# Kernel tuning notes

Measured on AMD Instinct MI355X. Metric: run time of the kernel, lower is better.

## Reference

```python
import jax, jax.numpy as jnp
import numpy as np

NUM_CAMS = 4
E = 256          # embed_dim
H_HEADS = 8      # num_heads
DH = E // H_HEADS
CIN = 64
FF = 4 * E
N_LAYERS = 2
EPS = 1e-5


def _layer_norm(x, g, b):
    mu = jnp.mean(x, axis=-1, keepdims=True)
    var = jnp.mean((x - mu) ** 2, axis=-1, keepdims=True)
    return (x - mu) * jax.lax.rsqrt(var + EPS) * g + b


def setup_inputs() -> dict:
    key = jax.random.key(0)
    ks = jax.random.split(key, 20)
    s = 0.02
    inp = {
        "features": jax.random.normal(ks[0], (NUM_CAMS, 2, CIN, 96, 96), jnp.float32),
        # 1x1 input projection conv
        "Wp": jax.random.normal(ks[1], (E, CIN), jnp.float32) * s,
        "bp": jnp.zeros((E,), jnp.float32),
        # per-layer attention params (stacked over 2 layers)
        "Wqkv": jax.random.normal(ks[2], (N_LAYERS, 3 * E, E), jnp.float32) * s,
        "bqkv": jnp.zeros((N_LAYERS, 3 * E), jnp.float32),
        "Wo": jax.random.normal(ks[3], (N_LAYERS, E, E), jnp.float32) * s,
        "bo": jnp.zeros((N_LAYERS, E), jnp.float32),
        # FFN
        "W1": jax.random.normal(ks[4], (N_LAYERS, FF, E), jnp.float32) * s,
        "b1": jnp.zeros((N_LAYERS, FF), jnp.float32),
        "W2": jax.random.normal(ks[5], (N_LAYERS, E, FF), jnp.float32) * s,
        "b2": jnp.zeros((N_LAYERS, E), jnp.float32),
        # LayerNorms
        "g1": jnp.ones((N_LAYERS, E), jnp.float32),
        "be1": jnp.zeros((N_LAYERS, E), jnp.float32),
        "g2": jnp.ones((N_LAYERS, E), jnp.float32),
        "be2": jnp.zeros((N_LAYERS, E), jnp.float32),
        # 1x1 output conv
        "Wout": jax.random.normal(ks[6], (CIN, E), jnp.float32) * s,
        "bout": jnp.zeros((CIN,), jnp.float32),
    }
    return inp


def reference(features, Wp, bp, Wqkv, bqkv, Wo, bo, W1, b1, W2, b2,
              g1, be1, g2, be2, Wout, bout):
    n_cam, B, Cin, Hh, Ww = features.shape
    # 1x1 conv projection + rearrange to per-pixel sequences: [B*H*W, n_cam, E]
    x = jnp.einsum('nbchw,ec->bhwne', features, Wp) + bp
    x = x.reshape(B * Hh * Ww, n_cam, E)

    scale = 1.0 / jnp.sqrt(jnp.float32(DH))
    for i in range(N_LAYERS):
        # self-attention (post-norm encoder layer, dropout=identity in eval)
        qkv = x @ Wqkv[i].T + bqkv[i]                      # [N, S, 3E]
        q, k, v = jnp.split(qkv, 3, axis=-1)
        q = q.reshape(-1, n_cam, H_HEADS, DH)
        k = k.reshape(-1, n_cam, H_HEADS, DH)
        v = v.reshape(-1, n_cam, H_HEADS, DH)
        scores = jnp.einsum('nqhd,nkhd->nhqk', q, k) * scale
        attn = jax.nn.softmax(scores, axis=-1)
        sa = jnp.einsum('nhqk,nkhd->nqhd', attn, v).reshape(-1, n_cam, E)
        sa = sa @ Wo[i].T + bo[i]
        x = _layer_norm(x + sa, g1[i], be1[i])
        # FFN (ReLU activation, default)
        ff = jax.nn.relu(x @ W1[i].T + b1[i]) @ W2[i].T + b2[i]
        x = _layer_norm(x + ff, g2[i], be2[i])

    # mean over cameras, back to [B, C, H, W] via 1x1 output conv
    fused = x.mean(axis=1).reshape(B, Hh, Ww, E)
    out = jnp.einsum('bhwe,ce->bchw', fused, Wout) + bout[None, :, None, None]
    return out
```

## Files before the change

### kernel.cpp

```cpp
#include <hip/hip_runtime.h>
#include <cstdint>
#include <cstddef>


typedef __bf16 bf16;
typedef __bf16 bf16x8 __attribute__((ext_vector_type(8)));
typedef __bf16 bf16x4 __attribute__((ext_vector_type(4)));
typedef float  f32x4  __attribute__((ext_vector_type(4)));

__device__ __forceinline__ void async_copy16(const void* g, void* l)
{
    __builtin_amdgcn_global_load_lds(
        (__attribute__((address_space(1))) void*)g,
        (__attribute__((address_space(3))) void*)l,
        16, 0, 0);
}

__global__ void pack_all_k(const float* __restrict__ s0, const float* __restrict__ s1,
                           const float* __restrict__ s2, const float* __restrict__ s3,
                           const float* __restrict__ s4,
                           bf16* __restrict__ d0, bf16* __restrict__ d1,
                           bf16* __restrict__ d2, bf16* __restrict__ d3,
                           bf16* __restrict__ d4)
{
    const int i = blockIdx.x * 256 + threadIdx.x;
    if (i < 393216)       d0[i] = (bf16)s0[i];
    else if (i < 524288)  d1[i - 393216] = (bf16)s1[i - 393216];
    else if (i < 1048576) d2[i - 524288] = (bf16)s2[i - 524288];
    else if (i < 1572864) d3[i - 1048576] = (bf16)s3[i - 1048576];
    else                  d4[i - 1572864] = (bf16)s4[i - 1572864];
}

__global__ __launch_bounds__(256) void feat_pack_k(const float* __restrict__ feat,
                                                   bf16* __restrict__ Xf)
{
    __shared__ float ft[64][68];

    const int tid  = threadIdx.x;
    const int camb = blockIdx.y;
    const int cam  = camb >> 1;
    const int b    = camb & 1;
    const int hw0  = blockIdx.x * 64;

    const float* fb = feat + (size_t)camb * 64 * 9216 + hw0;
#pragma unroll
    for (int rep = 0; rep < 16; ++rep) {
        const int idx = rep * 256 + tid;
        const int c = idx >> 6, p = idx & 63;
        ft[p][c] = fb[(size_t)c * 9216 + p];
    }
    __syncthreads();

    const int pbase = b * 9216 + hw0;
#pragma unroll
    for (int rep = 0; rep < 2; ++rep) {
        const int idx = rep * 256 + tid;
        const int p = idx >> 3, cc = idx & 7;
        const f32x4 a = *(const f32x4*)(&ft[p][cc * 8]);
        const f32x4 c4 = *(const f32x4*)(&ft[p][cc * 8 + 4]);
        bf16x8 v;
#pragma unroll
        for (int i = 0; i < 4; ++i) { v[i] = (bf16)a[i]; v[4 + i] = (bf16)c4[i]; }
        const size_t t = (size_t)(pbase + p) * 4 + cam;
        *(bf16x8*)(Xf + t * 64 + cc * 8) = v;
    }
}

template <bool RELU>
__global__ __launch_bounds__(256, 2) void gemm_bt(
    const bf16* __restrict__ A, const bf16* __restrict__ B,
    const float* __restrict__ bias, bf16* __restrict__ C,
    int N, int K)
{
    __shared__ __align__(16) bf16 As[128 * 64];
    __shared__ __align__(16) bf16 Bs[128 * 64];

    const int tid  = threadIdx.x;
    const int lane = tid & 63;
    const int wv   = tid >> 6;
    const int wm   = wv >> 1;
    const int wn   = wv & 1;
    const int bm   = blockIdx.y * 128;
    const int bn   = blockIdx.x * 128;

    const int r8  = lane >> 3;
    const int p8  = lane & 7;
    const int gch = p8 ^ r8;

    const int quad = lane >> 4;
    const int l16  = lane & 15;

    f32x4 acc[4][4] = {};

    for (int k0 = 0; k0 < K; k0 += 64) {
#pragma unroll
        for (int inst = 0; inst < 4; ++inst) {
            const int row = wv * 32 + inst * 8 + r8;
            const bf16* ga = A + (size_t)(bm + row) * K + (k0 + gch * 8);
            const bf16* gb = B + (size_t)(bn + row) * K + (k0 + gch * 8);
            async_copy16(ga, (char*)As + (wv * 4 + inst) * 1024);
            async_copy16(gb, (char*)Bs + (wv * 4 + inst) * 1024);
        }
        __syncthreads();

#pragma unroll
        for (int kk = 0; kk < 2; ++kk) {
            bf16x8 af[4], bfr[4];
            const int lch = kk * 4 + quad;
#pragma unroll
            for (int i = 0; i < 4; ++i) {
                const int m = wm * 64 + i * 16 + l16;
                af[i] = *(const bf16x8*)((const char*)As + (m * 8 + (lch ^ (m & 7))) * 16);
                const int n = wn * 64 + i * 16 + l16;
                bfr[i] = *(const bf16x8*)((const char*)Bs + (n * 8 + (lch ^ (n & 7))) * 16);
            }
#pragma unroll
            for (int i = 0; i < 4; ++i)
#pragma unroll
                for (int j = 0; j < 4; ++j)
                    acc[i][j] = __builtin_amdgcn_mfma_f32_16x16x32_bf16(
                        af[i], bfr[j], acc[i][j], 0, 0, 0);
        }
        __syncthreads();
    }

#pragma unroll
    for (int j = 0; j < 4; ++j) {
        const int n = bn + wn * 64 + j * 16 + l16;
        const float bv = bias[n];
#pragma unroll
        for (int i = 0; i < 4; ++i) {
            const int mb = bm + wm * 64 + i * 16 + quad * 4;
#pragma unroll
            for (int r = 0; r < 4; ++r) {
                float v = acc[i][j][r] + bv;
                if (RELU) v = fmaxf(v, 0.f);
                C[(size_t)(mb + r) * N + n] = (bf16)v;
            }
        }
    }
}

__global__ __launch_bounds__(256, 2) void gemm_ln_k(
    const bf16* __restrict__ A, const bf16* __restrict__ B,
    const float* __restrict__ bias, const bf16* __restrict__ Xres,
    const float* __restrict__ gam, const float* __restrict__ bet,
    bf16* __restrict__ Xout, int K)
{
    __shared__ __align__(16) bf16 S[24576];
    __shared__ float2 red[128][2];

    const int tid  = threadIdx.x;
    const int lane = tid & 63;
    const int wv   = tid >> 6;
    const int wm   = wv >> 1;
    const int wn   = wv & 1;
    const int bm   = blockIdx.x * 128;
    const int quad = lane >> 4;
    const int l16  = lane & 15;

    f32x4 acc[4][8] = {};

    for (int k0 = 0; k0 < K; k0 += 64) {
#pragma unroll
        for (int s = 0; s < 12; ++s) {
            const int L   = s * 256 + tid;
            const int row = L >> 3;
            const int gch = (L & 7) ^ (row & 7);
            const bf16* g = (row < 128)
                ? A + (size_t)(bm + row) * K + (k0 + gch * 8)
                : B + (size_t)(row - 128) * K + (k0 + gch * 8);
            async_copy16(g, (char*)S + (size_t)L * 16);
        }
        __syncthreads();

#pragma unroll
        for (int kk = 0; kk < 2; ++kk) {
            const int lch = kk * 4 + quad;
            bf16x8 af[4], bfr[8];
#pragma unroll
            for (int i = 0; i < 4; ++i) {
                const int m = wm * 64 + i * 16 + l16;
                af[i] = *(const bf16x8*)((const char*)S + (m * 8 + (lch ^ (m & 7))) * 16);
            }
#pragma unroll
            for (int j = 0; j < 8; ++j) {
                const int n = wn * 128 + j * 16 + l16;
                bfr[j] = *(const bf16x8*)((const char*)S + ((128 + n) * 8 + (lch ^ (n & 7))) * 16);
            }
#pragma unroll
            for (int i = 0; i < 4; ++i)
#pragma unroll
                for (int j = 0; j < 8; ++j)
                    acc[i][j] = __builtin_amdgcn_mfma_f32_16x16x32_bf16(
                        af[i], bfr[j], acc[i][j], 0, 0, 0);
        }
        __syncthreads();
    }

    float bv[8], gv[8], bev[8];
#pragma unroll
    for (int j = 0; j < 8; ++j) {
        const int n = wn * 128 + j * 16 + l16;
        bv[j] = bias[n]; gv[j] = gam[n]; bev[j] = bet[n];
    }

#pragma unroll
    for (int i = 0; i < 4; ++i) {
#pragma unroll
        for (int r = 0; r < 4; ++r) {
            const int rl  = wm * 64 + i * 16 + quad * 4 + r;
            const size_t row = (size_t)(bm + rl);
            float s1 = 0.f, s2 = 0.f;
#pragma unroll
            for (int j = 0; j < 8; ++j) {
                const int n = wn * 128 + j * 16 + l16;
                const float v = acc[i][j][r] + bv[j] + (float)Xres[row * 256 + n];
                acc[i][j][r] = v;
                s1 += v; s2 += v * v;
            }
#pragma unroll
            for (int off = 1; off < 16; off <<= 1) {
                s1 += __shfl_xor(s1, off, 64);
                s2 += __shfl_xor(s2, off, 64);
            }
            if (l16 == 0) red[rl][wn] = make_float2(s1, s2);
        }
    }
    __syncthreads();

#pragma unroll
    for (int i = 0; i < 4; ++i) {
#pragma unroll
        for (int r = 0; r < 4; ++r) {
            const int rl = wm * 64 + i * 16 + quad * 4 + r;
            const float2 p0 = red[rl][0], p1 = red[rl][1];
            const float mu  = (p0.x + p1.x) * (1.f / 256.f);
            const float ex2 = (p0.y + p1.y) * (1.f / 256.f);
            const float rstd = rsqrtf(fmaxf(ex2 - mu * mu, 0.f) + 1e-5f);
            const size_t row = (size_t)(bm + rl);
#pragma unroll
            for (int j = 0; j < 8; ++j) {
                const int n = wn * 128 + j * 16 + l16;
                Xout[row * 256 + n] = (bf16)((acc[i][j][r] - mu) * rstd * gv[j] + bev[j]);
            }
        }
    }
}

__device__ __forceinline__ void ffn_stage(int s, const bf16* __restrict__ W1,
                                          const bf16* __restrict__ W2,
                                          char* buf, int tid)
{
    const int hc = s >> 3;
    const int q  = s & 7;
    if (q < 4) {
#pragma unroll
        for (int it = 0; it < 4; ++it) {
            const int L = it * 256 + tid;
            const int row = L >> 3, psl = L & 7;
            const int c = psl ^ (row & 7);
            async_copy16(W1 + (size_t)(hc * 128 + row) * 256 + q * 64 + c * 8,
                         buf + (size_t)L * 16);
        }
    } else {
#pragma unroll
        for (int it = 0; it < 4; ++it) {
            const int L = it * 256 + tid;
            const int r128 = L >> 3, psl = L & 7;
            const int g = psl ^ (r128 & 7);
            const int n = r128 * 2 + (g >> 2);
            const int c = g & 3;
            async_copy16(W2 + (size_t)n * 1024 + hc * 128 + (q - 4) * 32 + c * 8,
                         buf + (size_t)L * 16);
        }
    }
}

__global__ __launch_bounds__(256, 2) void ffn_fused_k(
    const bf16* __restrict__ X,
    const bf16* __restrict__ W1, const float* __restrict__ b1,
    const bf16* __restrict__ W2, const float* __restrict__ b2,
    const float* __restrict__ gam, const float* __restrict__ bet,
    bf16* __restrict__ Xout)
{
    __shared__ __align__(16) char smem[81920];
    bf16* Xs = (bf16*)smem;
    bf16* Ts = (bf16*)(smem + 32768);
    float2 (*red)[2] = (float2 (*)[2])(void*)(smem + 32768);
    char* stg = smem + 49152;

    const int tid  = threadIdx.x;
    const int lane = tid & 63;
    const int wv   = tid >> 6;
    const int wm   = wv >> 1;
    const int wn   = wv & 1;
    const int quad = lane >> 4;
    const int l16  = lane & 15;
    const int bm   = blockIdx.x * 64;

#pragma unroll
    for (int it = 0; it < 8; ++it) {
        const int L = it * 256 + tid;
        const int row = L >> 5, slot = L & 31;
        const int gch = (slot & 24) | ((slot ^ row) & 7);
        async_copy16(X + (size_t)(bm + row) * 256 + gch * 8,
                     (char*)Xs + (size_t)L * 16);
    }
    ffn_stage(0, W1, W2, stg, tid);
    __syncthreads();

    f32x4 acc2[2][8] = {};

#pragma unroll 1
    for (int hc = 0; hc < 8; ++hc) {
        f32x4 accA[2][4] = {};

#pragma unroll
        for (int q = 0; q < 4; ++q) {
            const int s = hc * 8 + q;
            const char* cur = stg + (size_t)(s & 1) * 16384;
            ffn_stage(s + 1, W1, W2, stg + (size_t)((s + 1) & 1) * 16384, tid);
#pragma unroll
            for (int kk = 0; kk < 2; ++kk) {
                const int ch = kk * 4 + quad;
                const int gc = q * 8 + ch;
                bf16x8 af[2], bfr[4];
#pragma unroll
                for (int i = 0; i < 2; ++i) {
                    const int m  = wm * 32 + i * 16 + l16;
                    const int sl = (gc & 24) | ((gc ^ m) & 7);
                    af[i] = *(const bf16x8*)((const char*)Xs + (m * 32 + sl) * 16);
                }
#pragma unroll
                for (int j = 0; j < 4; ++j) {
                    const int n  = wn * 64 + j * 16 + l16;
                    const int sl = ch ^ (n & 7);
                    bfr[j] = *(const bf16x8*)(cur + (n * 8 + sl) * 16);
                }
#pragma unroll
                for (int i = 0; i < 2; ++i)
#pragma unroll
                    for (int j = 0; j < 4; ++j)
                        accA[i][j] = __builtin_amdgcn_mfma_f32_16x16x32_bf16(
                            af[i], bfr[j], accA[i][j], 0, 0, 0);
            }
            __syncthreads();
        }

#pragma unroll
        for (int j = 0; j < 4; ++j) {
            const int h  = wn * 64 + j * 16 + l16;
            const float bb = b1[hc * 128 + h];
            const int g  = h >> 3;
#pragma unroll
            for (int i = 0; i < 2; ++i)
#pragma unroll
                for (int r = 0; r < 4; ++r) {
                    const int m  = wm * 32 + i * 16 + quad * 4 + r;
                    const int sl = (g & 8) | ((g ^ m) & 7);
                    const float v = fmaxf(accA[i][j][r] + bb, 0.f);
                    *((bf16*)((char*)Ts + (m * 16 + sl) * 16 + (h & 7) * 2)) = (bf16)v;
                }
        }
        __syncthreads();

#pragma unroll
        for (int q = 0; q < 4; ++q) {
            const int s = hc * 8 + 4 + q;
            const char* cur = stg + (size_t)(s & 1) * 16384;
            if (s < 63)
                ffn_stage(s + 1, W1, W2, stg + (size_t)((s + 1) & 1) * 16384, tid);
            const int tc = q * 4 + quad;
            bf16x8 af[2], bfr[8];
#pragma unroll
            for (int i = 0; i < 2; ++i) {
                const int m  = wm * 32 + i * 16 + l16;
                const int sl = (tc & 8) | ((tc ^ m) & 7);
                af[i] = *(const bf16x8*)((const char*)Ts + (m * 16 + sl) * 16);
            }
#pragma unroll
            for (int j = 0; j < 8; ++j) {
                const int n  = wn * 128 + j * 16 + l16;
                const int sl = (((n & 1) * 4 + quad) ^ ((n >> 1) & 7)) & 7;
                bfr[j] = *(const bf16x8*)(cur + ((n >> 1) * 8 + sl) * 16);
            }
#pragma unroll
            for (int i = 0; i < 2; ++i)
#pragma unroll
                for (int j = 0; j < 8; ++j)
                    acc2[i][j] = __builtin_amdgcn_mfma_f32_16x16x32_bf16(
                        af[i], bfr[j], acc2[i][j], 0, 0, 0);
            __syncthreads();
        }
    }

    float bv[8], gv[8], bev[8];
#pragma unroll
    for (int j = 0; j < 8; ++j) {
        const int n = wn * 128 + j * 16 + l16;
        bv[j] = b2[n]; gv[j] = gam[n]; bev[j] = bet[n];
    }

#pragma unroll
    for (int i = 0; i < 2; ++i) {
#pragma unroll
        for (int r = 0; r < 4; ++r) {
            const int rl = wm * 32 + i * 16 + quad * 4 + r;
            float s1 = 0.f, s2 = 0.f;
#pragma unroll
            for (int j = 0; j < 8; ++j) {
                const int n  = wn * 128 + j * 16 + l16;
                const int gc = n >> 3;
                const int sl = (gc & 24) | ((gc ^ rl) & 7);
                const float xr = (float)*((const bf16*)((const char*)Xs +
                                   (rl * 32 + sl) * 16 + (n & 7) * 2));
                const float v = acc2[i][j][r] + bv[j] + xr;
                acc2[i][j][r] = v;
                s1 += v; s2 += v * v;
            }
#pragma unroll
            for (int off = 1; off < 16; off <<= 1) {
                s1 += __shfl_xor(s1, off, 64);
                s2 += __shfl_xor(s2, off, 64);
            }
            if (l16 == 0) red[rl][wn] = make_float2(s1, s2);
        }
    }
    __syncthreads();

#pragma unroll
    for (int i = 0; i < 2; ++i) {
#pragma unroll
        for (int r = 0; r < 4; ++r) {
            const int rl = wm * 32 + i * 16 + quad * 4 + r;
            const float2 p0 = red[rl][0], p1 = red[rl][1];
            const float mu  = (p0.x + p1.x) * (1.f / 256.f);
            const float ex2 = (p0.y + p1.y) * (1.f / 256.f);
            const float rstd = rsqrtf(fmaxf(ex2 - mu * mu, 0.f) + 1e-5f);
            const size_t row = (size_t)(bm + rl);
#pragma unroll
            for (int j = 0; j < 8; ++j) {
                const int n = wn * 128 + j * 16 + l16;
                Xout[row * 256 + n] = (bf16)((acc2[i][j][r] - mu) * rstd * gv[j] + bev[j]);
            }
        }
    }
}

__global__ __launch_bounds__(256) void attention_k(const bf16* __restrict__ QKV,
                                                   bf16* __restrict__ SA)
{
    __shared__ float qf[4][4][768];
    __shared__ float sc[4][8][4][4];

    const int tid  = threadIdx.x;
    const int wv   = tid >> 6;
    const int lane = tid & 63;
    const int s    = blockIdx.x * 4 + wv;

    const bf16* base = QKV + (size_t)s * 4 * 768;
#pragma unroll
    for (int it = 0; it < 6; ++it) {
        const int idx = it * 64 + lane;
        const bf16x8 v = *(const bf16x8*)(base + idx * 8);
        const int tok = idx / 96;
        const int e   = (idx % 96) * 8;
        f32x4 f0, f1;
#pragma unroll
        for (int i = 0; i < 4; ++i) { f0[i] = (float)v[i]; f1[i] = (float)v[4 + i]; }
        *(f32x4*)(&qf[wv][tok][e])     = f0;
        *(f32x4*)(&qf[wv][tok][e + 4]) = f1;
    }
    __syncthreads();

#pragma unroll
    for (int rep = 0; rep < 2; ++rep) {
        const int t = rep * 64 + lane;
        const int h = t >> 4, i = (t >> 2) & 3, j = t & 3;
        const float* q = &qf[wv][i][h * 32];
        const float* k = &qf[wv][j][256 + h * 32];
        float a = 0.f;
#pragma unroll
        for (int dd = 0; dd < 32; ++dd) {
            const int d = (dd + lane) & 31;
            a += q[d] * k[d];
        }
        sc[wv][h][i][j] = a * 0.17677669529663687f;
    }
    __syncthreads();

    if (lane < 32) {
        const int h = lane >> 2, i = lane & 3;
        float s0 = sc[wv][h][i][0], s1 = sc[wv][h][i][1];
        float s2 = sc[wv][h][i][2], s3 = sc[wv][h][i][3];
        float m = fmaxf(fmaxf(s0, s1), fmaxf(s2, s3));
        float e0 = expf(s0 - m), e1 = expf(s1 - m);
        float e2 = expf(s2 - m), e3 = expf(s3 - m);
        float inv = 1.f / (e0 + e1 + e2 + e3);
        sc[wv][h][i][0] = e0 * inv;
        sc[wv][h][i][1] = e1 * inv;
        sc[wv][h][i][2] = e2 * inv;
        sc[wv][h][i][3] = e3 * inv;
    }
    __syncthreads();

    const int h = lane >> 3;
#pragma unroll
    for (int i = 0; i < 4; ++i) {
        f32x4 a = {0.f, 0.f, 0.f, 0.f};
#pragma unroll
        for (int j = 0; j < 4; ++j) {
            const float p = sc[wv][h][i][j];
            const f32x4 v = *(const f32x4*)(&qf[wv][j][512 + lane * 4]);
#pragma unroll
            for (int q = 0; q < 4; ++q) a[q] += p * v[q];
        }
        bf16x4 o;
#pragma unroll
        for (int q = 0; q < 4; ++q) o[q] = (bf16)a[q];
        *(bf16x4*)(SA + (size_t)(s * 4 + i) * 256 + lane * 4) = o;
    }
}

__global__ __launch_bounds__(256) void out_proj_k(const bf16* __restrict__ X,
                                                  const float* __restrict__ Wout,
                                                  const float* __restrict__ bout,
                                                  float* __restrict__ out)
{
    __shared__ float fused[16][260];
    const int tid = threadIdx.x;
    const int p0  = blockIdx.x * 16;

#pragma unroll
    for (int it = 0; it < 16; ++it) {
        const int idx = it * 256 + tid;
        const int pix = idx >> 8, e = idx & 255;
        const size_t base = (size_t)(p0 + pix) * 1024 + e;
        const float s = (float)X[base] + (float)X[base + 256] +
                        (float)X[base + 512] + (float)X[base + 768];
        fused[pix][e] = s * 0.25f;
    }
    __syncthreads();

    const int pix = tid & 15;
    const int c0  = tid >> 4;
    const int p   = p0 + pix;
    const int b   = p / 9216;
    const int hw  = p % 9216;
#pragma unroll
    for (int it = 0; it < 4; ++it) {
        const int c = it * 16 + c0;
        const float* w = Wout + c * 256;
        float acc = bout[c];
#pragma unroll 8
        for (int e = 0; e < 256; ++e) acc += fused[pix][e] * w[e];
        out[((size_t)b * 64 + c) * 9216 + hw] = acc;
    }
}

extern "C" void kernel_launch(void* const* d_in, const int* in_sizes, int n_in,
                              void* d_out, int out_size, void* d_ws, size_t ws_size,
                              hipStream_t stream)
{
    const float* features = (const float*)d_in[0];
    const float* Wp   = (const float*)d_in[1];
    const float* bp   = (const float*)d_in[2];
    const float* Wqkv = (const float*)d_in[3];
    const float* bqkv = (const float*)d_in[4];
    const float* Wo   = (const float*)d_in[5];
    const float* bo   = (const float*)d_in[6];
    const float* W1   = (const float*)d_in[7];
    const float* b1   = (const float*)d_in[8];
    const float* W2   = (const float*)d_in[9];
    const float* b2   = (const float*)d_in[10];
    const float* g1   = (const float*)d_in[11];
    const float* be1  = (const float*)d_in[12];
    const float* g2   = (const float*)d_in[13];
    const float* be2  = (const float*)d_in[14];
    const float* Wout = (const float*)d_in[15];
    const float* bout = (const float*)d_in[16];
    float* out = (float*)d_out;

    char* ws = (char*)d_ws;
    bf16* X   = (bf16*)(ws);
    bf16* QKV = (bf16*)(ws + 37748736ull);
    bf16* SAb = (bf16*)(ws + 150994944ull);
    bf16* Xf  = (bf16*)(ws + 188743680ull);
    bf16* WpB = (bf16*)(ws + 198180864ull);
    bf16* Wb  = (bf16*)(ws + 226492416ull);

    bf16* WqkvB = Wb;
    bf16* WoB   = Wb + 393216;
    bf16* W1B   = Wb + 524288;
    bf16* W2B   = Wb + 1048576;

    pack_all_k<<<6208, 256, 0, stream>>>(Wqkv, Wo, W1, W2, Wp,
                                         WqkvB, WoB, W1B, W2B, WpB);

    feat_pack_k<<<dim3(144, 8), 256, 0, stream>>>(features, Xf);
    gemm_bt<false><<<dim3(2, 576), 256, 0, stream>>>(Xf, WpB, bp, X, 256, 64);

    for (int l = 0; l < 2; ++l) {
        gemm_bt<false><<<dim3(6, 576), 256, 0, stream>>>(
            X, WqkvB + l * 196608, bqkv + l * 768, QKV, 768, 256);
        attention_k<<<4608, 256, 0, stream>>>(QKV, SAb);
        gemm_ln_k<<<576, 256, 0, stream>>>(
            SAb, WoB + l * 65536, bo + l * 256, X,
            g1 + l * 256, be1 + l * 256, X, 256);
        ffn_fused_k<<<1152, 256, 0, stream>>>(
            X, W1B + l * 262144, b1 + l * 1024,
            W2B + l * 262144, b2 + l * 256,
            g2 + l * 256, be2 + l * 256, X);
    }

    out_proj_k<<<1152, 256, 0, stream>>>(X, Wout, bout, out);
}
```

Before: 648.1 us.

## Pre-pack W2 into MFMA fragment layout and read it directly from global

Adds a pack kernel that reorders W2 into per-lane MFMA B-fragment order. The FFN kernel then reads W2 fragments straight from global/L2 instead of staging them through LDS, which removes the W2 async copies and their per-step barriers. The bias/ReLU write into the hidden tile is folded into the last W1 step. The cost is per-wave global loads on the critical path, which rely on L2 hits, in place of shared LDS reuse across waves.

```diff
diff --git a/kernel.cpp b/kernel.cpp
--- a/kernel.cpp
+++ b/kernel.cpp
@@ -29,6 +29,24 @@
     else if (i < 1048576) d2[i - 524288] = (bf16)s2[i - 524288];
     else if (i < 1572864) d3[i - 1048576] = (bf16)s3[i - 1048576];
     else                  d4[i - 1572864] = (bf16)s4[i - 1572864];
+}
+
+__global__ void pack_w2f_k(const float* __restrict__ W2, bf16* __restrict__ W2F)
+{
+    const int g  = blockIdx.x * 256 + threadIdx.x;
+    const int l  = g >> 15;
+    const int e  = g & 32767;
+    const int nt   = e >> 11;
+    const int rem  = e & 2047;
+    const int kc   = rem >> 6;
+    const int lane = rem & 63;
+    const int row  = nt * 16 + (lane & 15);
+    const int col  = kc * 32 + (lane >> 4) * 8;
+    const float* src = W2 + (size_t)l * 262144;
+    bf16x8 v;
+#pragma unroll
+    for (int q = 0; q < 8; ++q) v[q] = (bf16)src[(size_t)row * 1024 + col + q];
+    *(bf16x8*)(W2F + (size_t)l * 262144 + (size_t)e * 8) = v;
 }
 
 __global__ __launch_bounds__(256) void feat_pack_k(const float* __restrict__ feat,
@@ -248,39 +266,26 @@
     }
 }
 
-__device__ __forceinline__ void ffn_stage(int s, const bf16* __restrict__ W1,
-                                          const bf16* __restrict__ W2,
-                                          char* buf, int tid)
-{
-    const int hc = s >> 3;
-    const int q  = s & 7;
-    if (q < 4) {
-#pragma unroll
-        for (int it = 0; it < 4; ++it) {
-            const int L = it * 256 + tid;
-            const int row = L >> 3, psl = L & 7;
-            const int c = psl ^ (row & 7);
-            async_copy16(W1 + (size_t)(hc * 128 + row) * 256 + q * 64 + c * 8,
-                         buf + (size_t)L * 16);
-        }
-    } else {
-#pragma unroll
-        for (int it = 0; it < 4; ++it) {
-            const int L = it * 256 + tid;
-            const int r128 = L >> 3, psl = L & 7;
-            const int g = psl ^ (r128 & 7);
-            const int n = r128 * 2 + (g >> 2);
-            const int c = g & 3;
-            async_copy16(W2 + (size_t)n * 1024 + hc * 128 + (q - 4) * 32 + c * 8,
-                         buf + (size_t)L * 16);
-        }
+__device__ __forceinline__ void ffn_stage_w1(int st, const bf16* __restrict__ W1,
+                                             char* stg, int tid)
+{
+    char* buf = stg + (size_t)(st & 1) * 16384;
+    const int hc = st >> 2;
+    const int q  = st & 3;
+#pragma unroll
+    for (int it = 0; it < 4; ++it) {
+        const int L = it * 256 + tid;
+        const int row = L >> 3, psl = L & 7;
+        const int c = psl ^ (row & 7);
+        async_copy16(W1 + (size_t)(hc * 128 + row) * 256 + q * 64 + c * 8,
+                     buf + (size_t)L * 16);
     }
 }
 
 __global__ __launch_bounds__(256, 2) void ffn_fused_k(
     const bf16* __restrict__ X,
     const bf16* __restrict__ W1, const float* __restrict__ b1,
-    const bf16* __restrict__ W2, const float* __restrict__ b2,
+    const bf16* __restrict__ W2f, const float* __restrict__ b2,
     const float* __restrict__ gam, const float* __restrict__ bet,
     bf16* __restrict__ Xout)
 {
@@ -307,7 +312,7 @@
         async_copy16(X + (size_t)(bm + row) * 256 + gch * 8,
                      (char*)Xs + (size_t)L * 16);
     }
-    ffn_stage(0, W1, W2, stg, tid);
+    ffn_stage_w1(0, W1, stg, tid);
     __syncthreads();
 
     f32x4 acc2[2][8] = {};
@@ -318,9 +323,9 @@
 
 #pragma unroll
         for (int q = 0; q < 4; ++q) {
-            const int s = hc * 8 + q;
-            const char* cur = stg + (size_t)(s & 1) * 16384;
-            ffn_stage(s + 1, W1, W2, stg + (size_t)((s + 1) & 1) * 16384, tid);
+            const int st = hc * 4 + q;
+            if (st + 1 < 32) ffn_stage_w1(st + 1, W1, stg, tid);
+            const char* cur = stg + (size_t)(st & 1) * 16384;
 #pragma unroll
             for (int kk = 0; kk < 2; ++kk) {
                 const int ch = kk * 4 + quad;
@@ -345,33 +350,29 @@
                         accA[i][j] = __builtin_amdgcn_mfma_f32_16x16x32_bf16(
                             af[i], bfr[j], accA[i][j], 0, 0, 0);
             }
+            if (q == 3) {
+#pragma unroll
+                for (int j = 0; j < 4; ++j) {
+                    const int h  = wn * 64 + j * 16 + l16;
+                    const float bb = b1[hc * 128 + h];
+                    const int g  = h >> 3;
+#pragma unroll
+                    for (int i = 0; i < 2; ++i)
+#pragma unroll
+                        for (int r = 0; r < 4; ++r) {
+                            const int m  = wm * 32 + i * 16 + quad * 4 + r;
+                            const int sl = (g & 8) | ((g ^ m) & 7);
+                            const float v = fmaxf(accA[i][j][r] + bb, 0.f);
+                            *((bf16*)((char*)Ts + (m * 16 + sl) * 16 + (h & 7) * 2)) = (bf16)v;
+                        }
+                }
+            }
             __syncthreads();
         }
 
-#pragma unroll
-        for (int j = 0; j < 4; ++j) {
-            const int h  = wn * 64 + j * 16 + l16;
-            const float bb = b1[hc * 128 + h];
-            const int g  = h >> 3;
-#pragma unroll
-            for (int i = 0; i < 2; ++i)
-#pragma unroll
-                for (int r = 0; r < 4; ++r) {
-                    const int m  = wm * 32 + i * 16 + quad * 4 + r;
-                    const int sl = (g & 8) | ((g ^ m) & 7);
-                    const float v = fmaxf(accA[i][j][r] + bb, 0.f);
-                    *((bf16*)((char*)Ts + (m * 16 + sl) * 16 + (h & 7) * 2)) = (bf16)v;
-                }
-        }
-        __syncthreads();
-
-#pragma unroll
-        for (int q = 0; q < 4; ++q) {
-            const int s = hc * 8 + 4 + q;
-            const char* cur = stg + (size_t)(s & 1) * 16384;
-            if (s < 63)
-                ffn_stage(s + 1, W1, W2, stg + (size_t)((s + 1) & 1) * 16384, tid);
-            const int tc = q * 4 + quad;
+#pragma unroll 2
+        for (int kc = 0; kc < 4; ++kc) {
+            const int tc = kc * 4 + quad;
             bf16x8 af[2], bfr[8];
 #pragma unroll
             for (int i = 0; i < 2; ++i) {
@@ -379,11 +380,11 @@
                 const int sl = (tc & 8) | ((tc ^ m) & 7);
                 af[i] = *(const bf16x8*)((const char*)Ts + (m * 16 + sl) * 16);
             }
+            const int kcg = hc * 4 + kc;
 #pragma unroll
             for (int j = 0; j < 8; ++j) {
-                const int n  = wn * 128 + j * 16 + l16;
-                const int sl = (((n & 1) * 4 + quad) ^ ((n >> 1) & 7)) & 7;
-                bfr[j] = *(const bf16x8*)(cur + ((n >> 1) * 8 + sl) * 16);
+                const int nt = wn * 8 + j;
+                bfr[j] = *(const bf16x8*)(W2f + ((size_t)(nt * 32 + kcg) * 64 + lane) * 8);
             }
 #pragma unroll
             for (int i = 0; i < 2; ++i)
@@ -391,9 +392,10 @@
                 for (int j = 0; j < 8; ++j)
                     acc2[i][j] = __builtin_amdgcn_mfma_f32_16x16x32_bf16(
                         af[i], bfr[j], acc2[i][j], 0, 0, 0);
-            __syncthreads();
-        }
-    }
+        }
+    }
+
+    __syncthreads();
 
     float bv[8], gv[8], bev[8];
 #pragma unroll
@@ -588,15 +590,16 @@
     bf16* SAb = (bf16*)(ws + 150994944ull);
     bf16* Xf  = (bf16*)(ws + 188743680ull);
     bf16* WpB = (bf16*)(ws + 198180864ull);
+    bf16* W2F = (bf16*)(ws + 198213632ull);
     bf16* Wb  = (bf16*)(ws + 226492416ull);
 
     bf16* WqkvB = Wb;
     bf16* WoB   = Wb + 393216;
     bf16* W1B   = Wb + 524288;
-    bf16* W2B   = Wb + 1048576;
 
     pack_all_k<<<6208, 256, 0, stream>>>(Wqkv, Wo, W1, W2, Wp,
-                                         WqkvB, WoB, W1B, W2B, WpB);
+                                         WqkvB, WoB, W1B, Wb + 1048576, WpB);
+    pack_w2f_k<<<256, 256, 0, stream>>>(W2, W2F);
 
     feat_pack_k<<<dim3(144, 8), 256, 0, stream>>>(features, Xf);
     gemm_bt<false><<<dim3(2, 576), 256, 0, stream>>>(Xf, WpB, bp, X, 256, 64);
@@ -610,7 +613,7 @@
             g1 + l * 256, be1 + l * 256, X, 256);
         ffn_fused_k<<<1152, 256, 0, stream>>>(
             X, W1B + l * 262144, b1 + l * 1024,
-            W2B + l * 262144, b2 + l * 256,
+            W2F + l * 262144, b2 + l * 256,
             g2 + l * 256, be2 + l * 256, X);
     }
 
```

Result: slower. 661.8 us (+2.1%).
